# Optimization experiments

Hardware: AMD Instinct MI355X
Metric: run time of the kernel (lower is better)

Reference implementation:

```python
import jax, jax.numpy as jnp
import numpy as np

N_EMBD = 1024
N_HEAD = 16
HEAD_SIZE = N_EMBD // N_HEAD  # 64
B, T = 4, 2048

def setup_inputs() -> dict:
    key = jax.random.key(0)
    k1, k2, k3, k4 = jax.random.split(key, 4)
    x = jax.random.normal(k1, (B, T, N_EMBD), dtype=jnp.float32)
    # weights stored as [in, out]; torch Linear does x @ W.T with W [out,in]
    w_qkv = jax.random.normal(k2, (N_EMBD, 3 * N_EMBD), dtype=jnp.float32) * (N_EMBD ** -0.5)
    w_proj = jax.random.normal(k3, (N_EMBD, N_EMBD), dtype=jnp.float32) * (N_EMBD ** -0.5)
    b_proj = jax.random.normal(k4, (N_EMBD,), dtype=jnp.float32) * 0.01
    return {"x": x, "w_qkv": w_qkv, "w_proj": w_proj, "b_proj": b_proj}

def reference(x, w_qkv, w_proj, b_proj):
    Bx, Tx, C = x.shape
    H, D = N_HEAD, HEAD_SIZE
    qkv = x @ w_qkv                               # [B,T,3C]
    q, k, v = jnp.split(qkv, 3, axis=-1)
    q = q.reshape(Bx, Tx, H, D).transpose(0, 2, 1, 3)  # [B,H,T,D]
    k = k.reshape(Bx, Tx, H, D).transpose(0, 2, 1, 3)
    v = v.reshape(Bx, Tx, H, D).transpose(0, 2, 1, 3)
    att = jnp.einsum('bhqd,bhkd->bhqk', q, k) * (D ** -0.5)  # [B,H,T,T]
    causal = jnp.tril(jnp.ones((Tx, Tx), dtype=bool))
    att = jnp.where(causal[None, None], att, -jnp.inf)
    att = jax.nn.softmax(att, axis=-1)
    out = jnp.einsum('bhqk,bhkd->bhqd', att, v)   # [B,H,T,D]
    out = out.transpose(0, 2, 1, 3).reshape(Bx, Tx, H * D)
    return out @ w_proj + b_proj
```

## Files before the change

### kernel.cpp

```cpp
#include <hip/hip_runtime.h>
#include <hip/hip_bf16.h>
#include <stdint.h>
#include <math.h>


typedef __attribute__((ext_vector_type(8))) short short8;
typedef __attribute__((ext_vector_type(4))) float f32x4;

#define LOG2E 1.44269504088896340736f
#define QSCALE 0.18033688011112042f

__device__ int g_isf32;

__device__ __forceinline__ void gl16(const void* g, void* l) {
  __builtin_amdgcn_global_load_lds(
      (const __attribute__((address_space(1))) unsigned int*)g,
      (__attribute__((address_space(3))) unsigned int*)l, 16, 0, 0);
}

__device__ __forceinline__ short f2bf(float f) {
  __hip_bfloat16 h = __float2bfloat16(f);
  return *reinterpret_cast<short*>(&h);
}
__device__ __forceinline__ float bf2f(short s) {
  __hip_bfloat16 h = *reinterpret_cast<__hip_bfloat16*>(&s);
  return __bfloat162float(h);
}
__device__ __forceinline__ short8 pack8(f32x4 lo, f32x4 hi) {
  short8 r;
#pragma unroll
  for (int e = 0; e < 4; ++e) { r[e] = f2bf(lo[e]); r[4 + e] = f2bf(hi[e]); }
  return r;
}

__device__ __forceinline__ unsigned cvtpk(float a, float b) {
  unsigned r;
  asm("v_cvt_pk_bf16_f32 %0, %1, %2" : "=v"(r) : "v"(a), "v"(b));
  return r;
}

__device__ __forceinline__ float dpp_sum16(float x) {
  int i;
  i = __builtin_amdgcn_update_dpp(0, __builtin_bit_cast(int, x), 0xB1, 0xF, 0xF, true);
  x += __builtin_bit_cast(float, i);
  i = __builtin_amdgcn_update_dpp(0, __builtin_bit_cast(int, x), 0x4E, 0xF, 0xF, true);
  x += __builtin_bit_cast(float, i);
  i = __builtin_amdgcn_update_dpp(0, __builtin_bit_cast(int, x), 0x141, 0xF, 0xF, true);
  x += __builtin_bit_cast(float, i);
  i = __builtin_amdgcn_update_dpp(0, __builtin_bit_cast(int, x), 0x140, 0xF, 0xF, true);
  x += __builtin_bit_cast(float, i);
  return x;
}

__global__ __launch_bounds__(256) void detect_dtype(const unsigned short* w) {
  __shared__ int cnt;
  if (threadIdx.x == 0) cnt = 0;
  __syncthreads();
  const unsigned short* p = w + (long)blockIdx.x * 49152;
  int c = 0;
  for (int i = threadIdx.x; i < 49152; i += 256)
    if (((p[i] >> 7) & 0xFF) == 0xFF) c++;
  atomicAdd(&cnt, c);
  __syncthreads();
  if (threadIdx.x == 0) g_isf32 = (cnt > 8) ? 1 : 0;
}

__global__ __launch_bounds__(256) void cvt_x(const void* __restrict__ src,
                                             short* __restrict__ dst) {
  const long i = ((long)blockIdx.x * 256 + threadIdx.x) * 8;
  if (g_isf32) {
    const float* s = (const float*)src + i;
    *(short8*)(dst + i) = pack8(*(const f32x4*)s, *(const f32x4*)(s + 4));
  } else {
    *(short8*)(dst + i) = *(const short8*)((const short*)src + i);
  }
}

template <int MODE>
__global__ __launch_bounds__(512, 2) void gemm_bt(
    const short* __restrict__ A, const short* __restrict__ Bt,
    const void* __restrict__ bias, void* __restrict__ C,
    short* __restrict__ vt, int M, int N, int K)
{
  __shared__ __align__(16) short As[3][16384];
  __shared__ __align__(16) short Bs[3][8192];
  const int tid  = threadIdx.x;
  const int lane = tid & 63;
  const int wave = tid >> 6;
  const int quad = lane >> 4;
  const int l16  = lane & 15;
  const int wm = (wave >> 1) * 64;
  const int wn = (wave & 1) * 64;

  const int gx = (int)gridDim.x;
  const int nwg = gx * (int)gridDim.y;
  int lb = (int)blockIdx.y * gx + (int)blockIdx.x;
  if ((nwg & 7) == 0) lb = (lb & 7) * (nwg >> 3) + (lb >> 3);
  const long m0 = (long)(lb / gx) * 256;
  const long n0 = (long)(lb % gx) * 128;

  int isf32 = 0;
  if (MODE == 1) {
    isf32 = g_isf32;
    asm volatile("s_waitcnt vmcnt(0) lgkmcnt(0)" ::: "memory");
  }

  f32x4 acc[4][4] = {};

  const int srow = tid >> 3;
  const int scol = ((tid & 7) ^ (srow & 7)) * 8;
  const short* Ag = A  + (m0 + srow) * (long)K + scol;
  const short* Bg = Bt + (n0 + srow) * (long)K + scol;
  const long rs64 = (long)64 * K;

  const int x7  = l16 & 7;
  const int xo0 = ((0 + quad) ^ x7) * 16;
  const int xo1 = ((4 + quad) ^ x7) * 16;
  const int aRow = (wm + l16) * 128;
  const int bRow = (wn + l16) * 128;

  auto STAGE_HALF = [&](int t2, int h) {
    const int bb = t2 % 3;
    const long k0 = (long)t2 << 6;
    gl16(Ag + k0 + (h * 2 + 0) * rs64, (char*)As[bb] + (h * 2 + 0) * 8192 + tid * 16);
    gl16(Ag + k0 + (h * 2 + 1) * rs64, (char*)As[bb] + (h * 2 + 1) * 8192 + tid * 16);
    gl16(Bg + k0 + h * rs64,           (char*)Bs[bb] + h * 8192 + tid * 16);
  };

  const int nt = K >> 6;
  STAGE_HALF(0, 0); STAGE_HALF(0, 1);
  STAGE_HALF(1, 0); STAGE_HALF(1, 1);

  for (int t = 0; t < nt; ++t) {
    if (t + 1 < nt) { asm volatile("s_waitcnt vmcnt(6)" ::: "memory"); }
    else            { asm volatile("s_waitcnt vmcnt(0)" ::: "memory"); }
    __builtin_amdgcn_sched_barrier(0);
    __builtin_amdgcn_s_barrier();
    __builtin_amdgcn_sched_barrier(0);

    const char* Ab = (const char*)As[t % 3];
    const char* Bb = (const char*)Bs[t % 3];

#pragma unroll
    for (int ph = 0; ph < 2; ++ph) {
      const int xo = ph ? xo1 : xo0;
      short8 af[4], bfv[4];
#pragma unroll
      for (int i = 0; i < 4; ++i)
        af[i] = *(const short8*)(Ab + aRow + i * 2048 + xo);
#pragma unroll
      for (int j = 0; j < 4; ++j)
        bfv[j] = *(const short8*)(Bb + bRow + j * 2048 + xo);
      if (t + 2 < nt) STAGE_HALF(t + 2, ph);
      __builtin_amdgcn_s_setprio(1);
#pragma unroll
      for (int i = 0; i < 4; ++i)
#pragma unroll
        for (int j = 0; j < 4; ++j)
          acc[i][j] = __builtin_amdgcn_mfma_f32_16x16x32_bf16(af[i], bfv[j], acc[i][j], 0, 0, 0);
      __builtin_amdgcn_s_setprio(0);
      if (ph == 0) {
        __builtin_amdgcn_s_barrier();
        __builtin_amdgcn_sched_barrier(0);
      }
    }
  }

#pragma unroll
  for (int j = 0; j < 4; ++j) {
    const long col = n0 + wn + j * 16 + l16;
    if (MODE == 2 && col >= 2048) {
      const long hd = col - 2048;
      const long bb = (m0 + wm) >> 11;
      const long tb = (m0 + wm) & 2047;
      short* vrow = vt + ((bb * 16 + (hd >> 6)) * 64 + (hd & 63)) * 2048 + tb;
#pragma unroll
      for (int ip = 0; ip < 2; ++ip)
#pragma unroll
        for (int r = 0; r < 4; ++r)
          *(unsigned*)&vrow[ip * 32 + 2 * (quad * 4 + r)] =
              cvtpk(acc[2 * ip][j][r], acc[2 * ip + 1][j][r]);
    } else {
      float bv = 0.f;
      if (MODE == 1)
        bv = isf32 ? ((const float*)bias)[col] : bf2f(((const short*)bias)[col]);
#pragma unroll
      for (int i = 0; i < 4; ++i) {
        const long row0 = m0 + wm + i * 16 + quad * 4;
#pragma unroll
        for (int r = 0; r < 4; ++r) {
          const long row = row0 + r;
          const float val = acc[i][j][r] + bv;
          if (MODE == 2) {
            const float vq = (col < 1024) ? val * QSCALE : val;
            ((short*)C)[row * 2048 + col] = f2bf(vq);
          } else {
            if (isf32) ((float*)C)[row * (long)N + col] = val;
            else       ((short*)C)[row * (long)N + col] = f2bf(val);
          }
        }
      }
    }
  }
}

__global__ __launch_bounds__(256) void transpose64(
    const void* __restrict__ src, short* __restrict__ dst, int R, int C)
{
  __shared__ __align__(16) short tile[64][72];
  const int isf32 = g_isf32;
  const int tid = threadIdx.x;
  const long r0 = (long)blockIdx.y * 64;
  const long c0 = (long)blockIdx.x * 64;
#pragma unroll
  for (int it = 0; it < 2; ++it) {
    int idx = it * 256 + tid;
    int rr = idx >> 3, ch = idx & 7;
    const long off = (r0 + rr) * C + c0 + ch * 8;
    short8 v;
    if (isf32) {
      const float* s = (const float*)src + off;
      v = pack8(*(const f32x4*)s, *(const f32x4*)(s + 4));
    } else {
      v = *(const short8*)((const short*)src + off);
    }
    *(short8*)&tile[rr][ch * 8] = v;
  }
  __syncthreads();
#pragma unroll
  for (int it = 0; it < 2; ++it) {
    int idx = it * 256 + tid;
    int cc = idx >> 3, ch = idx & 7;
    short8 v;
#pragma unroll
    for (int jj = 0; jj < 8; ++jj) v[jj] = tile[ch * 8 + jj][cc];
    *(short8*)&dst[(c0 + cc) * R + r0 + ch * 8] = v;
  }
}

__global__ __launch_bounds__(256) void attn_fwd(
    const short* __restrict__ qk, const short* __restrict__ vt,
    short* __restrict__ out)
{
  __shared__ __align__(16) short Ks[2][64][32];
  __shared__ __align__(16) short Vs[2][64][32];
  __shared__ __align__(16) unsigned Pw[4][16][36];
  const int tid = threadIdx.x;
  const int lane = tid & 63, wave = tid >> 6;
  const int quad = lane >> 4, l16 = lane & 15;
  const int bh = blockIdx.x;
  const int b = bh >> 4, h = bh & 15;
  const int py = blockIdx.y;

  const int sr = tid >> 2;
  const int scz = (tid & 3) ^ (sr & 3);
  const short* kg = qk + (long)b * 2048 * 2048 + 1024 + h * 64 + (long)sr * 2048 + scz * 8;
  const short* vg = vt + ((long)bh * 64 + sr) * 2048 + scz * 8;

  const int fx = (quad ^ (l16 & 3)) * 16;

  for (int hseg = 0; hseg < 2; ++hseg) {
    const int jq = hseg ? (31 - py) : py;
    const int qbase = jq * 64 + wave * 16;

    const short* qp = qk + ((long)(b * 2048 + qbase + l16)) * 2048 + h * 64 + quad * 8;
    const short8 aq0 = *(const short8*)qp;
    const short8 aq1 = *(const short8*)(qp + 32);

    f32x4 o[4] = {};
    float l_run[4] = {0.f, 0.f, 0.f, 0.f};

    for (int kt = 0; kt < jq; ++kt) {
      const int k0 = kt * 64;

      __syncthreads();
      gl16(kg + (long)k0 * 2048,      (char*)Ks + tid * 16);
      gl16(kg + (long)k0 * 2048 + 32, (char*)Ks + 4096 + tid * 16);
      gl16(vg + k0,                   (char*)Vs + tid * 16);
      gl16(vg + k0 + 32,              (char*)Vs + 4096 + tid * 16);
      __syncthreads();

      f32x4 s[4];
#pragma unroll
      for (int c = 0; c < 4; ++c) {
        short8 kf0 = *(const short8*)((const char*)&Ks[0][c * 16 + l16][0] + fx);
        short8 kf1 = *(const short8*)((const char*)&Ks[1][c * 16 + l16][0] + fx);
        f32x4 z = {};
        z = __builtin_amdgcn_mfma_f32_16x16x32_bf16(aq0, kf0, z, 0, 0, 0);
        z = __builtin_amdgcn_mfma_f32_16x16x32_bf16(aq1, kf1, z, 0, 0, 0);
        s[c] = z;
      }

      float p[4][4];
#pragma unroll
      for (int c = 0; c < 4; ++c)
#pragma unroll
        for (int r = 0; r < 4; ++r) {
          p[c][r] = __builtin_amdgcn_exp2f(s[c][r]);
          l_run[r] += p[c][r];
        }
#pragma unroll
      for (int r = 0; r < 4; ++r) {
        Pw[wave][quad * 4 + r][l16]      = cvtpk(p[0][r], p[1][r]);
        Pw[wave][quad * 4 + r][16 + l16] = cvtpk(p[2][r], p[3][r]);
      }

      {
        short8 pf0 = *(const short8*)&Pw[wave][l16][quad * 4];
        short8 pf1 = *(const short8*)&Pw[wave][l16][16 + quad * 4];
#pragma unroll
        for (int i = 0; i < 4; ++i) {
          short8 vf0 = *(const short8*)((const char*)&Vs[0][i * 16 + l16][0] + fx);
          o[i] = __builtin_amdgcn_mfma_f32_16x16x32_bf16(pf0, vf0, o[i], 0, 0, 0);
          short8 vf1 = *(const short8*)((const char*)&Vs[1][i * 16 + l16][0] + fx);
          o[i] = __builtin_amdgcn_mfma_f32_16x16x32_bf16(pf1, vf1, o[i], 0, 0, 0);
        }
      }
    }

    {
      const int k0 = jq * 64;

      __syncthreads();
      gl16(kg + (long)k0 * 2048,      (char*)Ks + tid * 16);
      gl16(kg + (long)k0 * 2048 + 32, (char*)Ks + 4096 + tid * 16);
      gl16(vg + k0,                   (char*)Vs + tid * 16);
      gl16(vg + k0 + 32,              (char*)Vs + 4096 + tid * 16);
      __syncthreads();

      float p[4][4];
#pragma unroll
      for (int c = 0; c < 4; ++c) {
        if (c > wave) {
#pragma unroll
          for (int r = 0; r < 4; ++r) p[c][r] = 0.f;
          continue;
        }
        short8 kf0 = *(const short8*)((const char*)&Ks[0][c * 16 + l16][0] + fx);
        short8 kf1 = *(const short8*)((const char*)&Ks[1][c * 16 + l16][0] + fx);
        f32x4 z = {};
        z = __builtin_amdgcn_mfma_f32_16x16x32_bf16(aq0, kf0, z, 0, 0, 0);
        z = __builtin_amdgcn_mfma_f32_16x16x32_bf16(aq1, kf1, z, 0, 0, 0);
        if (c == wave) {
#pragma unroll
          for (int r = 0; r < 4; ++r)
            z[r] = (l16 > quad * 4 + r) ? -1e30f : z[r];
        }
#pragma unroll
        for (int r = 0; r < 4; ++r) {
          p[c][r] = __builtin_amdgcn_exp2f(z[r]);
          l_run[r] += p[c][r];
        }
      }
#pragma unroll
      for (int r = 0; r < 4; ++r) {
        Pw[wave][quad * 4 + r][l16] = cvtpk(p[0][r], p[1][r]);
        if (wave >= 2)
          Pw[wave][quad * 4 + r][16 + l16] = cvtpk(p[2][r], p[3][r]);
      }

      {
        short8 pf0 = *(const short8*)&Pw[wave][l16][quad * 4];
#pragma unroll
        for (int i = 0; i < 4; ++i) {
          short8 vf0 = *(const short8*)((const char*)&Vs[0][i * 16 + l16][0] + fx);
          o[i] = __builtin_amdgcn_mfma_f32_16x16x32_bf16(pf0, vf0, o[i], 0, 0, 0);
        }
        if (wave >= 2) {
          short8 pf1 = *(const short8*)&Pw[wave][l16][16 + quad * 4];
#pragma unroll
          for (int i = 0; i < 4; ++i) {
            short8 vf1 = *(const short8*)((const char*)&Vs[1][i * 16 + l16][0] + fx);
            o[i] = __builtin_amdgcn_mfma_f32_16x16x32_bf16(pf1, vf1, o[i], 0, 0, 0);
          }
        }
      }
    }

#pragma unroll
    for (int r = 0; r < 4; ++r) l_run[r] = dpp_sum16(l_run[r]);
    float inv[4];
#pragma unroll
    for (int r = 0; r < 4; ++r) inv[r] = 1.0f / l_run[r];
    short* op = out + ((long)(b * 2048 + qbase + quad * 4)) * 1024 + h * 64;
#pragma unroll
    for (int i = 0; i < 4; ++i)
#pragma unroll
      for (int r = 0; r < 4; ++r)
        op[(long)r * 1024 + i * 16 + l16] = f2bf(o[i][r] * inv[r]);
  }
}

__global__ __launch_bounds__(256) void copy_out(const void* __restrict__ src,
                                                void* __restrict__ dst)
{
  const long n16 = g_isf32 ? 2097152L : 1048576L;
  const uint4* s = (const uint4*)src;
  uint4* d = (uint4*)dst;
  for (long i = (long)blockIdx.x * 256 + threadIdx.x; i < n16;
       i += (long)gridDim.x * 256)
    d[i] = s[i];
}

extern "C" void kernel_launch(void* const* d_in, const int* in_sizes, int n_in,
                              void* d_out, int out_size, void* d_ws, size_t ws_size,
                              hipStream_t stream)
{
  const void* x      = d_in[0];
  const void* w_qkv  = d_in[1];
  const void* w_proj = d_in[2];
  const void* b_proj = d_in[3];

  short* ws = (short*)d_ws;
  const bool planA = ws_size >= 67108864ULL;

  short* qk  = ws;
  short* vtp = ws + 16777216L;

  short *wqkvT, *attnb, *wprojT, *xbf;
  void*  projC;
  if (planA) {
    attnb  = ws + 25165824L;
    wqkvT  = attnb;
    wprojT = qk;
    xbf    = (short*)d_out;
    projC  = d_out;
  } else {
    wqkvT  = (short*)d_out;
    xbf    = (short*)d_out + 3145728L;
    attnb  = (short*)d_out;
    wprojT = vtp;
    projC  = qk;
  }

  detect_dtype<<<64, 256, 0, stream>>>((const unsigned short*)w_qkv);
  cvt_x<<<4096, 256, 0, stream>>>(x, xbf);
  transpose64<<<dim3(3072 / 64, 1024 / 64), 256, 0, stream>>>(w_qkv, wqkvT, 1024, 3072);
  gemm_bt<2><<<dim3(3072 / 128, 8192 / 256), 512, 0, stream>>>(
      xbf, wqkvT, nullptr, qk, vtp, 8192, 3072, 1024);
  attn_fwd<<<dim3(64, 16), 256, 0, stream>>>(qk, vtp, attnb);
  transpose64<<<dim3(1024 / 64, 1024 / 64), 256, 0, stream>>>(w_proj, wprojT, 1024, 1024);
  gemm_bt<1><<<dim3(1024 / 128, 8192 / 256), 512, 0, stream>>>(
      attnb, wprojT, b_proj, projC, nullptr, 8192, 1024, 1024);
  if (!planA)
    copy_out<<<2048, 256, 0, stream>>>(projC, d_out);
}
```

Baseline: 274.8 us.

## Pipeline attention K/V loads with triple buffering and 128-row query blocks

The attention kernel now uses 512-thread blocks of 8 waves that together cover 128 query rows. Each block shares one K/V tile load across twice as many query rows, halving K/V traffic per query. The K/V tiles go into a 3-stage shared-memory ring filled by async global-to-LDS loads issued two tiles ahead, with explicit vmcnt waits and a single barrier per tile in place of the old two-barrier synchronous load. This is meant to hide global-load latency behind the MFMA work, at the cost of more LDS per block, fewer blocks in the grid, and per-wave causal skipping that leaves some waves idle on diagonal tiles.

```diff
diff --git a/kernel.cpp b/kernel.cpp
--- a/kernel.cpp
+++ b/kernel.cpp
@@ -238,139 +238,108 @@
   }
 }
 
-__global__ __launch_bounds__(256) void attn_fwd(
+__global__ __launch_bounds__(512) void attn_fwd(
     const short* __restrict__ qk, const short* __restrict__ vt,
     short* __restrict__ out)
 {
-  __shared__ __align__(16) short Ks[2][64][32];
-  __shared__ __align__(16) short Vs[2][64][32];
-  __shared__ __align__(16) unsigned Pw[4][16][36];
+  __shared__ __align__(16) short Ks[3][2][64][32];
+  __shared__ __align__(16) short Vs[3][2][64][32];
+  __shared__ __align__(16) unsigned Pw[8][16][36];
   const int tid = threadIdx.x;
   const int lane = tid & 63, wave = tid >> 6;
   const int quad = lane >> 4, l16 = lane & 15;
   const int bh = blockIdx.x;
   const int b = bh >> 4, h = bh & 15;
-  const int py = blockIdx.y;
-
-  const int sr = tid >> 2;
-  const int scz = (tid & 3) ^ (sr & 3);
-  const short* kg = qk + (long)b * 2048 * 2048 + 1024 + h * 64 + (long)sr * 2048 + scz * 8;
-  const short* vg = vt + ((long)bh * 64 + sr) * 2048 + scz * 8;
+
+  const int shalf = tid >> 8;
+  const int srow  = (tid >> 2) & 63;
+  const int sc    = (tid & 3) ^ (srow & 3);
+  const short* kg = qk + (long)b * 2048 * 2048 + 1024 + h * 64
+                      + (long)srow * 2048 + shalf * 32 + sc * 8;
+  const short* vg = vt + ((long)bh * 64 + srow) * 2048 + shalf * 32 + sc * 8;
 
   const int fx = (quad ^ (l16 & 3)) * 16;
 
-  for (int hseg = 0; hseg < 2; ++hseg) {
-    const int jq = hseg ? (31 - py) : py;
-    const int qbase = jq * 64 + wave * 16;
-
-    const short* qp = qk + ((long)(b * 2048 + qbase + l16)) * 2048 + h * 64 + quad * 8;
+  for (int seg = 0; seg < 2; ++seg) {
+    const int s = seg ? (15 - (int)blockIdx.y) : (int)blockIdx.y;
+    const int nt = 2 * s + 2;
+    const int qb = s * 128 + wave * 16;
+    const int qlast = qb + 15;
+
+    if (seg) __syncthreads();
+
+    const short* qp = qk + ((long)(b * 2048 + qb + l16)) * 2048 + h * 64 + quad * 8;
     const short8 aq0 = *(const short8*)qp;
     const short8 aq1 = *(const short8*)(qp + 32);
 
+    gl16(kg,                    (char*)Ks[0] + tid * 16);
+    gl16(vg,                    (char*)Vs[0] + tid * 16);
+    gl16(kg + (long)64 * 2048,  (char*)Ks[1] + tid * 16);
+    gl16(vg + 64,               (char*)Vs[1] + tid * 16);
+
     f32x4 o[4] = {};
     float l_run[4] = {0.f, 0.f, 0.f, 0.f};
 
-    for (int kt = 0; kt < jq; ++kt) {
+    for (int kt = 0; kt < nt; ++kt) {
+      if (kt + 1 < nt) { asm volatile("s_waitcnt vmcnt(2)" ::: "memory"); }
+      else             { asm volatile("s_waitcnt vmcnt(0)" ::: "memory"); }
+      __builtin_amdgcn_sched_barrier(0);
+      __builtin_amdgcn_s_barrier();
+      __builtin_amdgcn_sched_barrier(0);
+      if (kt + 2 < nt) {
+        const int rb = (kt + 2) % 3;
+        gl16(kg + (long)((kt + 2) * 64) * 2048, (char*)Ks[rb] + tid * 16);
+        gl16(vg + (kt + 2) * 64,                (char*)Vs[rb] + tid * 16);
+      }
+
       const int k0 = kt * 64;
-
-      __syncthreads();
-      gl16(kg + (long)k0 * 2048,      (char*)Ks + tid * 16);
-      gl16(kg + (long)k0 * 2048 + 32, (char*)Ks + 4096 + tid * 16);
-      gl16(vg + k0,                   (char*)Vs + tid * 16);
-      gl16(vg + k0 + 32,              (char*)Vs + 4096 + tid * 16);
-      __syncthreads();
-
-      f32x4 s[4];
+      if (k0 > qlast) continue;
+      const int rb0 = kt % 3;
+      const bool full = (k0 + 63 <= qb);
+      const bool h2 = (k0 + 32 <= qlast);
+
+      float p[4][4];
 #pragma unroll
       for (int c = 0; c < 4; ++c) {
-        short8 kf0 = *(const short8*)((const char*)&Ks[0][c * 16 + l16][0] + fx);
-        short8 kf1 = *(const short8*)((const char*)&Ks[1][c * 16 + l16][0] + fx);
-        f32x4 z = {};
-        z = __builtin_amdgcn_mfma_f32_16x16x32_bf16(aq0, kf0, z, 0, 0, 0);
-        z = __builtin_amdgcn_mfma_f32_16x16x32_bf16(aq1, kf1, z, 0, 0, 0);
-        s[c] = z;
-      }
-
-      float p[4][4];
-#pragma unroll
-      for (int c = 0; c < 4; ++c)
-#pragma unroll
-        for (int r = 0; r < 4; ++r) {
-          p[c][r] = __builtin_amdgcn_exp2f(s[c][r]);
-          l_run[r] += p[c][r];
+        if (full || (k0 + c * 16 <= qlast)) {
+          short8 kf0 = *(const short8*)((const char*)&Ks[rb0][0][c * 16 + l16][0] + fx);
+          short8 kf1 = *(const short8*)((const char*)&Ks[rb0][1][c * 16 + l16][0] + fx);
+          f32x4 z = {};
+          z = __builtin_amdgcn_mfma_f32_16x16x32_bf16(aq0, kf0, z, 0, 0, 0);
+          z = __builtin_amdgcn_mfma_f32_16x16x32_bf16(aq1, kf1, z, 0, 0, 0);
+          if (!full) {
+#pragma unroll
+            for (int r = 0; r < 4; ++r)
+              z[r] = (k0 + c * 16 + l16 > qb + quad * 4 + r) ? -1e30f : z[r];
+          }
+#pragma unroll
+          for (int r = 0; r < 4; ++r) {
+            p[c][r] = __builtin_amdgcn_exp2f(z[r]);
+            l_run[r] += p[c][r];
+          }
+        } else {
+#pragma unroll
+          for (int r = 0; r < 4; ++r) p[c][r] = 0.f;
         }
+      }
 #pragma unroll
       for (int r = 0; r < 4; ++r) {
-        Pw[wave][quad * 4 + r][l16]      = cvtpk(p[0][r], p[1][r]);
-        Pw[wave][quad * 4 + r][16 + l16] = cvtpk(p[2][r], p[3][r]);
+        Pw[wave][quad * 4 + r][l16] = cvtpk(p[0][r], p[1][r]);
+        if (h2) Pw[wave][quad * 4 + r][16 + l16] = cvtpk(p[2][r], p[3][r]);
       }
 
       {
         short8 pf0 = *(const short8*)&Pw[wave][l16][quad * 4];
-        short8 pf1 = *(const short8*)&Pw[wave][l16][16 + quad * 4];
 #pragma unroll
         for (int i = 0; i < 4; ++i) {
-          short8 vf0 = *(const short8*)((const char*)&Vs[0][i * 16 + l16][0] + fx);
-          o[i] = __builtin_amdgcn_mfma_f32_16x16x32_bf16(pf0, vf0, o[i], 0, 0, 0);
-          short8 vf1 = *(const short8*)((const char*)&Vs[1][i * 16 + l16][0] + fx);
-          o[i] = __builtin_amdgcn_mfma_f32_16x16x32_bf16(pf1, vf1, o[i], 0, 0, 0);
-        }
-      }
-    }
-
-    {
-      const int k0 = jq * 64;
-
-      __syncthreads();
-      gl16(kg + (long)k0 * 2048,      (char*)Ks + tid * 16);
-      gl16(kg + (long)k0 * 2048 + 32, (char*)Ks + 4096 + tid * 16);
-      gl16(vg + k0,                   (char*)Vs + tid * 16);
-      gl16(vg + k0 + 32,              (char*)Vs + 4096 + tid * 16);
-      __syncthreads();
-
-      float p[4][4];
-#pragma unroll
-      for (int c = 0; c < 4; ++c) {
-        if (c > wave) {
-#pragma unroll
-          for (int r = 0; r < 4; ++r) p[c][r] = 0.f;
-          continue;
-        }
-        short8 kf0 = *(const short8*)((const char*)&Ks[0][c * 16 + l16][0] + fx);
-        short8 kf1 = *(const short8*)((const char*)&Ks[1][c * 16 + l16][0] + fx);
-        f32x4 z = {};
-        z = __builtin_amdgcn_mfma_f32_16x16x32_bf16(aq0, kf0, z, 0, 0, 0);
-        z = __builtin_amdgcn_mfma_f32_16x16x32_bf16(aq1, kf1, z, 0, 0, 0);
-        if (c == wave) {
-#pragma unroll
-          for (int r = 0; r < 4; ++r)
-            z[r] = (l16 > quad * 4 + r) ? -1e30f : z[r];
-        }
-#pragma unroll
-        for (int r = 0; r < 4; ++r) {
-          p[c][r] = __builtin_amdgcn_exp2f(z[r]);
-          l_run[r] += p[c][r];
-        }
-      }
-#pragma unroll
-      for (int r = 0; r < 4; ++r) {
-        Pw[wave][quad * 4 + r][l16] = cvtpk(p[0][r], p[1][r]);
-        if (wave >= 2)
-          Pw[wave][quad * 4 + r][16 + l16] = cvtpk(p[2][r], p[3][r]);
-      }
-
-      {
-        short8 pf0 = *(const short8*)&Pw[wave][l16][quad * 4];
-#pragma unroll
-        for (int i = 0; i < 4; ++i) {
-          short8 vf0 = *(const short8*)((const char*)&Vs[0][i * 16 + l16][0] + fx);
+          short8 vf0 = *(const short8*)((const char*)&Vs[rb0][0][i * 16 + l16][0] + fx);
           o[i] = __builtin_amdgcn_mfma_f32_16x16x32_bf16(pf0, vf0, o[i], 0, 0, 0);
         }
-        if (wave >= 2) {
+        if (h2) {
           short8 pf1 = *(const short8*)&Pw[wave][l16][16 + quad * 4];
 #pragma unroll
           for (int i = 0; i < 4; ++i) {
-            short8 vf1 = *(const short8*)((const char*)&Vs[1][i * 16 + l16][0] + fx);
+            short8 vf1 = *(const short8*)((const char*)&Vs[rb0][1][i * 16 + l16][0] + fx);
             o[i] = __builtin_amdgcn_mfma_f32_16x16x32_bf16(pf1, vf1, o[i], 0, 0, 0);
           }
         }
@@ -382,7 +351,7 @@
     float inv[4];
 #pragma unroll
     for (int r = 0; r < 4; ++r) inv[r] = 1.0f / l_run[r];
-    short* op = out + ((long)(b * 2048 + qbase + quad * 4)) * 1024 + h * 64;
+    short* op = out + ((long)(b * 2048 + qb + quad * 4)) * 1024 + h * 64;
 #pragma unroll
     for (int i = 0; i < 4; ++i)
 #pragma unroll
@@ -438,7 +407,7 @@
   transpose64<<<dim3(3072 / 64, 1024 / 64), 256, 0, stream>>>(w_qkv, wqkvT, 1024, 3072);
   gemm_bt<2><<<dim3(3072 / 128, 8192 / 256), 512, 0, stream>>>(
       xbf, wqkvT, nullptr, qk, vtp, 8192, 3072, 1024);
-  attn_fwd<<<dim3(64, 16), 256, 0, stream>>>(qk, vtp, attnb);
+  attn_fwd<<<dim3(64, 8), 512, 0, stream>>>(qk, vtp, attnb);
   transpose64<<<dim3(1024 / 64, 1024 / 64), 256, 0, stream>>>(w_proj, wprojT, 1024, 1024);
   gemm_bt<1><<<dim3(1024 / 128, 8192 / 256), 512, 0, stream>>>(
       attnb, wprojT, b_proj, projC, nullptr, 8192, 1024, 1024);
```

After: 279.7 us (median of 2 runs). About the same (+1.8%).
